# Kernel tuning notes

Measured on AMD Instinct MI355X. Metric: run time of the kernel, lower is better.

## Reference

```python
import jax, jax.numpy as jnp
import numpy as np

BETA = 0.25
EPS = 1e-10


def setup_inputs() -> dict:
    key = jax.random.key(0)
    k1, k2 = jax.random.split(key)
    B, D, K = 32768, 512, 8192
    a = jax.random.normal(k1, (B, D), dtype=jnp.float32)
    # torch init: uniform(-1/K, 1/K)
    codebook = jax.random.uniform(k2, (K, D), dtype=jnp.float32,
                                  minval=-1.0 / K, maxval=1.0 / K)
    return {"a": a, "codebook": codebook}


def reference(a, codebook):
    # a: [B, D], codebook: [K, D]
    B = a.shape[0]
    K = codebook.shape[0]
    # squared-distance via a2 + e2 - 2*a.E^T (no [B,K,D] intermediate)
    a2 = jnp.sum(a * a, axis=1, keepdims=True)            # [B, 1]
    e2 = jnp.sum(codebook * codebook, axis=1)[None, :]    # [1, K]
    dist = a2 + e2 - 2.0 * (a @ codebook.T)               # [B, K]
    idx = jnp.argmin(dist, axis=1)                        # [B] int
    z_q = codebook[idx]                                   # [B, D]
    # straight-through estimator
    z = a + jax.lax.stop_gradient(z_q - a)
    commit_loss = BETA * jnp.mean((a - jax.lax.stop_gradient(z_q)) ** 2)
    codebook_loss = jnp.mean((jax.lax.stop_gradient(a) - z_q) ** 2)
    # usage stats (no_grad in torch)
    usage = jnp.zeros((K,), a.dtype).at[idx].add(1.0) / B  # mean of one-hot
    perplexity = jnp.exp(-jnp.sum(usage * jnp.log(usage + EPS)))
    used_codes = jnp.sum(usage > 0).astype(a.dtype)
    usage_mean = jnp.mean(usage)
    return (idx, z, commit_loss, codebook_loss, perplexity, used_codes, usage_mean)
```

## Files before the change

### kernel.cpp

```cpp
#include <hip/hip_runtime.h>
#include <stdint.h>

#define D_DIM 512
#define EBFS 544
#define ESTRIDE 528
#define SPLIT_K 384
#define DELTA 8.0e-4f
#define MAXC 48

typedef unsigned long long u64;
typedef float f32x4 __attribute__((ext_vector_type(4)));
typedef short s16x8 __attribute__((ext_vector_type(8)));

static __device__ inline unsigned short f2bf(float x) {
  unsigned u = __float_as_uint(x);
  u = (u + 0x7FFFu + ((u >> 16) & 1u)) >> 16;
  return (unsigned short)u;
}
static __device__ inline unsigned mono(float f) {
  unsigned u = __float_as_uint(f);
  return (u & 0x80000000u) ? ~u : (u | 0x80000000u);
}
static __device__ inline float unmono(unsigned m) {
  return __uint_as_float((m & 0x80000000u) ? (m & 0x7FFFFFFFu) : ~m);
}

__global__ void k_init(int* __restrict__ counts, int K) {
  int i = blockIdx.x * blockDim.x + threadIdx.x;
  if (i < K) counts[i] = 0;
}

__global__ void k_rowsq(const float* __restrict__ X, float* __restrict__ out, int nrows) {
  int t = threadIdx.x;
  int row = blockIdx.x * 4 + (t >> 6);
  int l = t & 63;
  if (row >= nrows) return;
  int b = l >> 4;
  int L = l & 15;
  const float* p = X + (size_t)row * D_DIM + b * 128 + L;
  float v[8];
#pragma unroll
  for (int j = 0; j < 8; ++j) {
    float x = p[16 * j];
    float sq = x * x;
    asm volatile("" : "+v"(sq));
    v[j] = sq;
  }
  float s = ((v[0] + v[1]) + (v[2] + v[3])) + ((v[4] + v[5]) + (v[6] + v[7]));
  s += __shfl_xor(s, 8, 64);
  s += __shfl_xor(s, 4, 64);
  s += __shfl_xor(s, 2, 64);
  s += __shfl_xor(s, 1, 64);
  s += __shfl_xor(s, 16, 64);
  s += __shfl_xor(s, 32, 64);
  if (l == 0) out[row] = s;
}

__global__ void k_ebf(const float* __restrict__ E, unsigned short* __restrict__ Ebf, int n8) {
  int i = blockIdx.x * blockDim.x + threadIdx.x;
  if (i >= n8) return;
  int row = i >> 6;
  int ch = i & 63;
  const float4 f0 = *(const float4*)(E + (size_t)row * D_DIM + ch * 8);
  const float4 f1 = *(const float4*)(E + (size_t)row * D_DIM + ch * 8 + 4);
  s16x8 o;
  o[0] = (short)f2bf(f0.x); o[1] = (short)f2bf(f0.y);
  o[2] = (short)f2bf(f0.z); o[3] = (short)f2bf(f0.w);
  o[4] = (short)f2bf(f1.x); o[5] = (short)f2bf(f1.y);
  o[6] = (short)f2bf(f1.z); o[7] = (short)f2bf(f1.w);
  *(s16x8*)(Ebf + (size_t)row * EBFS + ch * 8) = o;
}

__global__ void k_eskew(const float* __restrict__ E, float* __restrict__ Es, int n4) {
  int i = blockIdx.x * blockDim.x + threadIdx.x;
  if (i >= n4) return;
  int row = i >> 7;
  int c = i & 127;
  float4 v = ((const float4*)(E + (size_t)row * D_DIM))[c];
  ((float4*)(Es + (size_t)row * ESTRIDE))[c] = v;
}

__global__ __launch_bounds__(512, 2) void k_screen(
    const float* __restrict__ A, const unsigned short* __restrict__ Ebf,
    const float* __restrict__ e2, int* __restrict__ cand_cnt,
    unsigned short* __restrict__ cand, int K) {
  __shared__ unsigned runmin[128];
  __shared__ unsigned cnt[128];
  __shared__ unsigned short list[128 * MAXC];
  __shared__ __align__(16) char Alds[128 * 1024];

  const int t = threadIdx.x;
  const int m0 = blockIdx.x * 128;

  if (t < 128) { runmin[t] = 0xFFFFFFFFu; cnt[t] = 0; }

  {
    int row = t >> 2;
    int s4 = t & 3;
    const float* ar = A + (size_t)(m0 + row) * D_DIM;
#pragma unroll
    for (int c = 0; c < 16; ++c) {
      int ch = s4 * 16 + c;
      float4 f0 = *(const float4*)(ar + ch * 8);
      float4 f1 = *(const float4*)(ar + ch * 8 + 4);
      s16x8 o;
      o[0] = (short)f2bf(f0.x); o[1] = (short)f2bf(f0.y);
      o[2] = (short)f2bf(f0.z); o[3] = (short)f2bf(f0.w);
      o[4] = (short)f2bf(f1.x); o[5] = (short)f2bf(f1.y);
      o[6] = (short)f2bf(f1.z); o[7] = (short)f2bf(f1.w);
      int off = ((row * 64 + ch) * 16) ^ ((row & 15) << 4);
      *(s16x8*)(Alds + off) = o;
    }
  }
  __syncthreads();

  const int lane = t & 63;
  const int wid = t >> 6;
  const int wm = wid >> 2;
  const int wn = wid & 3;
  const int l15 = lane & 15;
  const int lhi = lane >> 4;

  for (int n0 = 0; n0 < K; n0 += 128) {
    s16x8 bb0[16], bb1[16];
    {
      const unsigned short* B0 = Ebf + (size_t)(n0 + wn * 32 + l15) * EBFS + lhi * 8;
      const unsigned short* B1 = B0 + 16 * EBFS;
#pragma unroll
      for (int dk = 0; dk < 16; ++dk) {
        bb0[dk] = *(const s16x8*)(B0 + dk * 32);
        bb1[dk] = *(const s16x8*)(B1 + dk * 32);
      }
    }
    f32x4 acc[4][2];
#pragma unroll
    for (int r = 0; r < 4; ++r)
#pragma unroll
      for (int c = 0; c < 2; ++c) acc[r][c] = (f32x4){0.f, 0.f, 0.f, 0.f};
#pragma unroll
    for (int dk = 0; dk < 16; ++dk) {
      s16x8 af[4];
#pragma unroll
      for (int r = 0; r < 4; ++r) {
        int row = wm * 64 + r * 16 + l15;
        int off = ((row * 64 + dk * 4 + lhi) * 16) ^ ((row & 15) << 4);
        af[r] = *(const s16x8*)(Alds + off);
      }
#pragma unroll
      for (int r = 0; r < 4; ++r) {
        acc[r][0] = __builtin_amdgcn_mfma_f32_16x16x32_bf16(af[r], bb0[dk], acc[r][0], 0, 0, 0);
        acc[r][1] = __builtin_amdgcn_mfma_f32_16x16x32_bf16(af[r], bb1[dk], acc[r][1], 0, 0, 0);
      }
    }
    float e2c0 = e2[n0 + wn * 32 + l15];
    float e2c1 = e2[n0 + wn * 32 + 16 + l15];
#pragma unroll
    for (int r = 0; r < 4; ++r)
#pragma unroll
      for (int g = 0; g < 4; ++g) {
        float s0 = fmaf(-2.f, acc[r][0][g], e2c0);
        float s1 = fmaf(-2.f, acc[r][1][g], e2c1);
        int row = wm * 64 + r * 16 + lhi * 4 + g;
        float mn = fminf(s0, s1);
        mn = fminf(mn, __shfl_xor(mn, 1, 64));
        mn = fminf(mn, __shfl_xor(mn, 2, 64));
        mn = fminf(mn, __shfl_xor(mn, 4, 64));
        mn = fminf(mn, __shfl_xor(mn, 8, 64));
        if (l15 == 0) atomicMin(&runmin[row], mono(mn));
        float thr = unmono(runmin[row]) + DELTA;
        if (s0 <= thr) {
          unsigned p = atomicAdd(&cnt[row], 1u);
          if (p < MAXC) list[row * MAXC + p] = (unsigned short)(n0 + wn * 32 + l15);
        }
        if (s1 <= thr) {
          unsigned p = atomicAdd(&cnt[row], 1u);
          if (p < MAXC) list[row * MAXC + p] = (unsigned short)(n0 + wn * 32 + 16 + l15);
        }
      }
  }
  __syncthreads();
  {
    int row = t >> 2;
    unsigned c = cnt[row];
    if ((t & 3) == 0) cand_cnt[m0 + row] = (int)c;
    unsigned cc = c < MAXC ? c : MAXC;
    for (unsigned p = t & 3; p < cc; p += 4)
      cand[(size_t)(m0 + row) * MAXC + p] = list[row * MAXC + p];
  }
}

static __device__ inline u64 exact_pack(const float* __restrict__ ar,
                                        const float* __restrict__ er,
                                        float a2r, float e2k, int k) {
  float acc1 = 0.f, acc2 = 0.f;
  for (int d = 0; d < SPLIT_K; d += 4) {
    float4 a = *(const float4*)(ar + d);
    float4 e = *(const float4*)(er + d);
    acc1 = fmaf(a.x, e.x, acc1); acc1 = fmaf(a.y, e.y, acc1);
    acc1 = fmaf(a.z, e.z, acc1); acc1 = fmaf(a.w, e.w, acc1);
  }
  for (int d = SPLIT_K; d < D_DIM; d += 4) {
    float4 a = *(const float4*)(ar + d);
    float4 e = *(const float4*)(er + d);
    acc2 = fmaf(a.x, e.x, acc2); acc2 = fmaf(a.y, e.y, acc2);
    acc2 = fmaf(a.z, e.z, acc2); acc2 = fmaf(a.w, e.w, acc2);
  }
  float M = acc1 + acc2;
  float S = a2r + e2k;
  float s = fmaf(-2.f, M, S);
  return ((u64)mono(s) << 32) | (unsigned)k;
}

__global__ __launch_bounds__(256) void k_rescore(
    const float* __restrict__ A, const float* __restrict__ Eskew,
    const float* __restrict__ a2, const float* __restrict__ e2,
    const int* __restrict__ cand_cnt, const unsigned short* __restrict__ cand,
    float* __restrict__ out_idx, float* __restrict__ out_z,
    float* __restrict__ rowsum, int* __restrict__ counts, int K) {
  int lane = threadIdx.x & 63;
  int r = blockIdx.x * 4 + (threadIdx.x >> 6);
  int c = cand_cnt[r];
  const float* ar = A + (size_t)r * D_DIM;
  float a2r = a2[r];
  u64 best = ~0ULL;
  if (c <= MAXC) {
    if (lane < c) {
      int k = cand[(size_t)r * MAXC + lane];
      best = exact_pack(ar, Eskew + (size_t)k * ESTRIDE, a2r, e2[k], k);
    }
  } else {
    for (int k = lane; k < K; k += 64) {
      u64 p = exact_pack(ar, Eskew + (size_t)k * ESTRIDE, a2r, e2[k], k);
      if (p < best) best = p;
    }
  }
#pragma unroll
  for (int m = 1; m < 64; m <<= 1) {
    u64 o = __shfl_xor(best, m, 64);
    if (o < best) best = o;
  }
  int idx = (int)(unsigned)(best & 0xFFFFFFFFULL);

  const float4* pa = (const float4*)(ar) + lane * 2;
  const float4* pe = (const float4*)(Eskew + (size_t)idx * ESTRIDE) + lane * 2;
  float4* pz = (float4*)(out_z + (size_t)r * D_DIM) + lane * 2;
  float ls = 0.f;
#pragma unroll
  for (int q = 0; q < 2; ++q) {
    float4 a = pa[q];
    float4 e = pe[q];
    float4 z;
    z.x = a.x + (e.x - a.x);
    z.y = a.y + (e.y - a.y);
    z.z = a.z + (e.z - a.z);
    z.w = a.w + (e.w - a.w);
    pz[q] = z;
    float dx = a.x - e.x, dy = a.y - e.y, dz = a.z - e.z, dw = a.w - e.w;
    ls += dx * dx + dy * dy + dz * dz + dw * dw;
  }
#pragma unroll
  for (int m = 1; m < 64; m <<= 1) ls += __shfl_xor(ls, m, 64);
  if (lane == 0) {
    out_idx[r] = (float)idx;
    rowsum[r] = ls;
    atomicAdd(&counts[idx], 1);
  }
}

#define KTILE(D0, ACC)                                                          \
  {                                                                             \
    int r = t >> 2;                                                             \
    int c4 = (t & 3) << 2;                                                      \
    float4 va = *(const float4*)(A + (size_t)(m0 + r) * D_DIM + (D0) + c4);     \
    As[c4 + 0][r] = va.x; As[c4 + 1][r] = va.y;                                 \
    As[c4 + 2][r] = va.z; As[c4 + 3][r] = va.w;                                 \
    float4 vb = *(const float4*)(E + (size_t)(n0 + r) * D_DIM + (D0) + c4);     \
    Es[c4 + 0][r] = vb.x; Es[c4 + 1][r] = vb.y;                                 \
    Es[c4 + 2][r] = vb.z; Es[c4 + 3][r] = vb.w;                                 \
    __syncthreads();                                                            \
    _Pragma("unroll")                                                           \
    for (int dd = 0; dd < 16; ++dd) {                                           \
      float af[4], bf[8];                                                       \
      *(float4*)af = *(const float4*)(&As[dd][ty * 4]);                         \
      *(float4*)bf = *(const float4*)(&Es[dd][tx * 4]);                         \
      *(float4*)(bf + 4) = *(const float4*)(&Es[dd][64 + tx * 4]);              \
      _Pragma("unroll")                                                         \
      for (int i = 0; i < 4; ++i)                                               \
        _Pragma("unroll")                                                       \
        for (int j = 0; j < 8; ++j)                                             \
          ACC[i][j] = fmaf(af[i], bf[j], ACC[i][j]);                            \
    }                                                                           \
    __syncthreads();                                                            \
  }

__global__ __launch_bounds__(512) void k_argmin_f32(
    const float* __restrict__ A, const float* __restrict__ E,
    const float* __restrict__ a2, const float* __restrict__ e2,
    float* __restrict__ out_idx, int* __restrict__ idx_ws, int K) {
  __shared__ float As[16][128];
  __shared__ float Es[16][128];
  const int m0 = blockIdx.x * 128;
  const int t = threadIdx.x;
  const int tx = t & 15;
  const int ty = t >> 4;
  float a2l[4];
#pragma unroll
  for (int i = 0; i < 4; ++i) a2l[i] = a2[m0 + ty * 4 + i];
  u64 best[4];
#pragma unroll
  for (int i = 0; i < 4; ++i) best[i] = ~0ULL;
  for (int n0 = 0; n0 < K; n0 += 128) {
    float acc1[4][8], acc2[4][8];
#pragma unroll
    for (int i = 0; i < 4; ++i)
#pragma unroll
      for (int j = 0; j < 8; ++j) { acc1[i][j] = 0.f; acc2[i][j] = 0.f; }
    for (int d0 = 0; d0 < SPLIT_K; d0 += 16) KTILE(d0, acc1)
    for (int d0 = SPLIT_K; d0 < D_DIM; d0 += 16) KTILE(d0, acc2)
    float e2l[8];
#pragma unroll
    for (int j = 0; j < 8; ++j) {
      int cl = (j < 4) ? (tx * 4 + j) : (64 + tx * 4 + (j - 4));
      e2l[j] = e2[n0 + cl];
    }
#pragma unroll
    for (int i = 0; i < 4; ++i) {
#pragma unroll
      for (int j = 0; j < 8; ++j) {
        int cl = (j < 4) ? (tx * 4 + j) : (64 + tx * 4 + (j - 4));
        float S = a2l[i] + e2l[j];
        float m = acc1[i][j] + acc2[i][j];
        float s = fmaf(-2.f, m, S);
        u64 p = ((u64)mono(s) << 32) | (unsigned)(n0 + cl);
        if (p < best[i]) best[i] = p;
      }
    }
  }
#pragma unroll
  for (int m = 1; m < 16; m <<= 1) {
#pragma unroll
    for (int i = 0; i < 4; ++i) {
      u64 o = __shfl_xor(best[i], m, 64);
      if (o < best[i]) best[i] = o;
    }
  }
  if (tx == 0) {
#pragma unroll
    for (int i = 0; i < 4; ++i) {
      int row = m0 + ty * 4 + i;
      int idx = (int)(unsigned)(best[i] & 0xFFFFFFFFULL);
      out_idx[row] = (float)idx;
      idx_ws[row] = idx;
    }
  }
}

__global__ void k_gather(const float* __restrict__ A, const float* __restrict__ E,
                         const int* __restrict__ idx_ws,
                         float* __restrict__ out_z, float* __restrict__ rowsum,
                         int* __restrict__ counts) {
  int b = blockIdx.x;
  int t = threadIdx.x;
  int idx = idx_ws[b];
  const float4* pa = (const float4*)(A + (size_t)b * D_DIM);
  const float4* pe = (const float4*)(E + (size_t)idx * D_DIM);
  float4 a = pa[t];
  float4 e = pe[t];
  float4 z;
  z.x = a.x + (e.x - a.x);
  z.y = a.y + (e.y - a.y);
  z.z = a.z + (e.z - a.z);
  z.w = a.w + (e.w - a.w);
  ((float4*)(out_z + (size_t)b * D_DIM))[t] = z;
  float dx = a.x - e.x, dy = a.y - e.y, dz = a.z - e.z, dw = a.w - e.w;
  float ls = dx * dx + dy * dy + dz * dz + dw * dw;
#pragma unroll
  for (int off = 32; off > 0; off >>= 1) ls += __shfl_down(ls, off, 64);
  __shared__ float wsum[2];
  if ((t & 63) == 0) wsum[t >> 6] = ls;
  __syncthreads();
  if (t == 0) {
    rowsum[b] = wsum[0] + wsum[1];
    atomicAdd(&counts[idx], 1);
  }
}

__global__ void k_stats(const int* __restrict__ counts, const float* __restrict__ rowsum,
                        float* __restrict__ out_sc, int B, int K) {
  int t = threadIdx.x;
  double ent = 0.0, tot = 0.0, S = 0.0;
  int used = 0;
  for (int k = t; k < K; k += 256) {
    int c = counts[k];
    double u = (double)c / (double)B;
    ent += u * log(u + 1e-10);
    tot += u;
    used += (c > 0) ? 1 : 0;
  }
  for (int b = t; b < B; b += 256) S += (double)rowsum[b];
  __shared__ double se[256];
  __shared__ double st[256];
  __shared__ double ss[256];
  __shared__ int su[256];
  se[t] = ent; st[t] = tot; ss[t] = S; su[t] = used;
  __syncthreads();
  for (int s = 128; s > 0; s >>= 1) {
    if (t < s) { se[t] += se[t + s]; st[t] += st[t + s]; ss[t] += ss[t + s]; su[t] += su[t + s]; }
    __syncthreads();
  }
  if (t == 0) {
    double Sm = ss[0];
    double N = (double)B * (double)D_DIM;
    out_sc[0] = (float)(0.25 * Sm / N);
    out_sc[1] = (float)(Sm / N);
    out_sc[2] = (float)exp(-se[0]);
    out_sc[3] = (float)su[0];
    out_sc[4] = (float)(st[0] / (double)K);
  }
}

extern "C" void kernel_launch(void* const* d_in, const int* in_sizes, int n_in,
                              void* d_out, int out_size, void* d_ws, size_t ws_size,
                              hipStream_t stream) {
  const float* A = (const float*)d_in[0];
  const float* E = (const float*)d_in[1];
  const int B = in_sizes[0] / D_DIM;
  const int K = in_sizes[1] / D_DIM;

  float* out = (float*)d_out;
  float* out_idx = out;
  float* out_z = out + B;
  float* out_sc = out + B + (size_t)B * D_DIM;

  char* ws = (char*)d_ws;
  size_t off = 0;
  float* a2 = (float*)(ws + off); off += (size_t)B * 4;
  float* e2 = (float*)(ws + off); off += (size_t)K * 4;
  int* counts = (int*)(ws + off); off += (size_t)K * 4;
  float* rowsum = (float*)(ws + off); off += (size_t)B * 4;
  int* idx_ws = (int*)(ws + off); off += (size_t)B * 4;
  int* cand_cnt = (int*)(ws + off); off += (size_t)B * 4;
  unsigned short* cand = (unsigned short*)(ws + off); off += (size_t)B * MAXC * 2;
  unsigned short* Ebf = (unsigned short*)(ws + off); off += (size_t)K * EBFS * 2;
  float* Eskew = (float*)(ws + off); off += (size_t)K * ESTRIDE * 4;
  const size_t need = off;

  k_init<<<(K + 255) / 256, 256, 0, stream>>>(counts, K);
  k_rowsq<<<(B + 3) / 4, 256, 0, stream>>>(A, a2, B);
  k_rowsq<<<(K + 3) / 4, 256, 0, stream>>>(E, e2, K);

  if (ws_size >= need) {
    int n8 = K * D_DIM / 8;
    k_ebf<<<(n8 + 255) / 256, 256, 0, stream>>>(E, Ebf, n8);
    int n4 = K * D_DIM / 4;
    k_eskew<<<(n4 + 255) / 256, 256, 0, stream>>>(E, Eskew, n4);
    k_screen<<<B / 128, 512, 0, stream>>>(A, Ebf, e2, cand_cnt, cand, K);
    k_rescore<<<B / 4, 256, 0, stream>>>(A, Eskew, a2, e2, cand_cnt, cand,
                                         out_idx, out_z, rowsum, counts, K);
  } else {
    k_argmin_f32<<<B / 128, 512, 0, stream>>>(A, E, a2, e2, out_idx, idx_ws, K);
    k_gather<<<B, 128, 0, stream>>>(A, E, idx_ws, out_z, rowsum, counts);
  }
  k_stats<<<1, 256, 0, stream>>>(counts, rowsum, out_sc, B, K);
}
```

Baseline: 910.2 us.

## Double-buffer codebook fragment loads in screen kernel and fuse prep kernels

The screen kernel's main loop now splits each codebook tile's fragment loads into two halves. The next tile's first half is prefetched while the current tile's MFMAs run, to hide global load latency behind matrix math. The codebook bf16 conversion, fp32 padded copy and counts zeroing are merged into a single prep kernel, removing two launches and one read of the codebook. The loop now hardcodes 64 tiles (K=8192), and keeping two buffers live may raise register pressure under the 512x2 launch bound.

```diff
diff --git a/kernel.cpp b/kernel.cpp
--- a/kernel.cpp
+++ b/kernel.cpp
@@ -28,6 +28,27 @@
 __global__ void k_init(int* __restrict__ counts, int K) {
   int i = blockIdx.x * blockDim.x + threadIdx.x;
   if (i < K) counts[i] = 0;
+}
+
+__global__ void k_prep(const float* __restrict__ E, unsigned short* __restrict__ Ebf,
+                       float* __restrict__ Eskew, int* __restrict__ counts, int K) {
+  int i = blockIdx.x * blockDim.x + threadIdx.x;
+  if (i < K) counts[i] = 0;
+  if (i >= K * 64) return;
+  int row = i >> 6;
+  int ch = i & 63;
+  const float* src = E + (size_t)row * D_DIM + ch * 8;
+  float4 f0 = *(const float4*)(src);
+  float4 f1 = *(const float4*)(src + 4);
+  s16x8 o;
+  o[0] = (short)f2bf(f0.x); o[1] = (short)f2bf(f0.y);
+  o[2] = (short)f2bf(f0.z); o[3] = (short)f2bf(f0.w);
+  o[4] = (short)f2bf(f1.x); o[5] = (short)f2bf(f1.y);
+  o[6] = (short)f2bf(f1.z); o[7] = (short)f2bf(f1.w);
+  *(s16x8*)(Ebf + (size_t)row * EBFS + ch * 8) = o;
+  float* dst = Eskew + (size_t)row * ESTRIDE + ch * 8;
+  *(float4*)(dst) = f0;
+  *(float4*)(dst + 4) = f1;
 }
 
 __global__ void k_rowsq(const float* __restrict__ X, float* __restrict__ out, int nrows) {
@@ -56,29 +77,25 @@
   if (l == 0) out[row] = s;
 }
 
-__global__ void k_ebf(const float* __restrict__ E, unsigned short* __restrict__ Ebf, int n8) {
-  int i = blockIdx.x * blockDim.x + threadIdx.x;
-  if (i >= n8) return;
-  int row = i >> 6;
-  int ch = i & 63;
-  const float4 f0 = *(const float4*)(E + (size_t)row * D_DIM + ch * 8);
-  const float4 f1 = *(const float4*)(E + (size_t)row * D_DIM + ch * 8 + 4);
-  s16x8 o;
-  o[0] = (short)f2bf(f0.x); o[1] = (short)f2bf(f0.y);
-  o[2] = (short)f2bf(f0.z); o[3] = (short)f2bf(f0.w);
-  o[4] = (short)f2bf(f1.x); o[5] = (short)f2bf(f1.y);
-  o[6] = (short)f2bf(f1.z); o[7] = (short)f2bf(f1.w);
-  *(s16x8*)(Ebf + (size_t)row * EBFS + ch * 8) = o;
-}
-
-__global__ void k_eskew(const float* __restrict__ E, float* __restrict__ Es, int n4) {
-  int i = blockIdx.x * blockDim.x + threadIdx.x;
-  if (i >= n4) return;
-  int row = i >> 7;
-  int c = i & 127;
-  float4 v = ((const float4*)(E + (size_t)row * D_DIM))[c];
-  ((float4*)(Es + (size_t)row * ESTRIDE))[c] = v;
-}
+#define LOADH(BUF, P0, P1, DKB)                                                 \
+  _Pragma("unroll") for (int dk = 0; dk < 8; ++dk) {                            \
+    BUF[dk]     = *(const s16x8*)((P0) + (DKB + dk) * 32);                      \
+    BUF[8 + dk] = *(const s16x8*)((P1) + (DKB + dk) * 32);                      \
+  }
+
+#define MFMAH(BUF, DKB)                                                         \
+  _Pragma("unroll") for (int dk = 0; dk < 8; ++dk) {                            \
+    s16x8 af[4];                                                                \
+    _Pragma("unroll") for (int r = 0; r < 4; ++r) {                             \
+      int row = wm * 64 + r * 16 + l15;                                         \
+      int off = ((row * 64 + (DKB + dk) * 4 + lhi) * 16) ^ ((row & 15) << 4);   \
+      af[r] = *(const s16x8*)(Alds + off);                                      \
+    }                                                                           \
+    _Pragma("unroll") for (int r = 0; r < 4; ++r) {                             \
+      acc[r][0] = __builtin_amdgcn_mfma_f32_16x16x32_bf16(af[r], BUF[dk], acc[r][0], 0, 0, 0);      \
+      acc[r][1] = __builtin_amdgcn_mfma_f32_16x16x32_bf16(af[r], BUF[8 + dk], acc[r][1], 0, 0, 0);  \
+    }                                                                           \
+  }
 
 __global__ __launch_bounds__(512, 2) void k_screen(
     const float* __restrict__ A, const unsigned short* __restrict__ Ebf,
@@ -121,37 +138,30 @@
   const int l15 = lane & 15;
   const int lhi = lane >> 4;
 
-  for (int n0 = 0; n0 < K; n0 += 128) {
-    s16x8 bb0[16], bb1[16];
-    {
-      const unsigned short* B0 = Ebf + (size_t)(n0 + wn * 32 + l15) * EBFS + lhi * 8;
-      const unsigned short* B1 = B0 + 16 * EBFS;
-#pragma unroll
-      for (int dk = 0; dk < 16; ++dk) {
-        bb0[dk] = *(const s16x8*)(B0 + dk * 32);
-        bb1[dk] = *(const s16x8*)(B1 + dk * 32);
-      }
-    }
+  const unsigned short* Bbase = Ebf + (size_t)(wn * 32 + l15) * EBFS + lhi * 8;
+
+  s16x8 bufA[16], bufB[16];
+  LOADH(bufA, Bbase, Bbase + 16 * EBFS, 0)
+
+  for (int tile = 0; tile < 64; ++tile) {
+    const int n0 = tile * 128;
+    const unsigned short* P0 = Bbase + (size_t)n0 * EBFS;
+    const unsigned short* P1 = P0 + 16 * EBFS;
+
     f32x4 acc[4][2];
 #pragma unroll
     for (int r = 0; r < 4; ++r)
 #pragma unroll
       for (int c = 0; c < 2; ++c) acc[r][c] = (f32x4){0.f, 0.f, 0.f, 0.f};
-#pragma unroll
-    for (int dk = 0; dk < 16; ++dk) {
-      s16x8 af[4];
-#pragma unroll
-      for (int r = 0; r < 4; ++r) {
-        int row = wm * 64 + r * 16 + l15;
-        int off = ((row * 64 + dk * 4 + lhi) * 16) ^ ((row & 15) << 4);
-        af[r] = *(const s16x8*)(Alds + off);
-      }
-#pragma unroll
-      for (int r = 0; r < 4; ++r) {
-        acc[r][0] = __builtin_amdgcn_mfma_f32_16x16x32_bf16(af[r], bb0[dk], acc[r][0], 0, 0, 0);
-        acc[r][1] = __builtin_amdgcn_mfma_f32_16x16x32_bf16(af[r], bb1[dk], acc[r][1], 0, 0, 0);
-      }
-    }
+
+    LOADH(bufB, P0, P1, 8)
+    MFMAH(bufA, 0)
+    if (tile < 63) {
+      const unsigned short* N0 = P0 + (size_t)128 * EBFS;
+      LOADH(bufA, N0, N0 + 16 * EBFS, 0)
+    }
+    MFMAH(bufB, 8)
+
     float e2c0 = e2[n0 + wn * 32 + l15];
     float e2c1 = e2[n0 + wn * 32 + 16 + l15];
 #pragma unroll
@@ -445,19 +455,17 @@
   float* Eskew = (float*)(ws + off); off += (size_t)K * ESTRIDE * 4;
   const size_t need = off;
 
-  k_init<<<(K + 255) / 256, 256, 0, stream>>>(counts, K);
   k_rowsq<<<(B + 3) / 4, 256, 0, stream>>>(A, a2, B);
   k_rowsq<<<(K + 3) / 4, 256, 0, stream>>>(E, e2, K);
 
   if (ws_size >= need) {
-    int n8 = K * D_DIM / 8;
-    k_ebf<<<(n8 + 255) / 256, 256, 0, stream>>>(E, Ebf, n8);
-    int n4 = K * D_DIM / 4;
-    k_eskew<<<(n4 + 255) / 256, 256, 0, stream>>>(E, Eskew, n4);
+    int np = K * 64;
+    k_prep<<<(np + 255) / 256, 256, 0, stream>>>(E, Ebf, Eskew, counts, K);
     k_screen<<<B / 128, 512, 0, stream>>>(A, Ebf, e2, cand_cnt, cand, K);
     k_rescore<<<B / 4, 256, 0, stream>>>(A, Eskew, a2, e2, cand_cnt, cand,
                                          out_idx, out_z, rowsum, counts, K);
   } else {
+    k_init<<<(K + 255) / 256, 256, 0, stream>>>(counts, K);
     k_argmin_f32<<<B / 128, 512, 0, stream>>>(A, E, a2, e2, out_idx, idx_ws, K);
     k_gather<<<B, 128, 0, stream>>>(A, E, idx_ws, out_z, rowsum, counts);
   }
```

Result: faster. 870.6 us (-4.3%).
